# Kernel optimization log

Measured on AMD Instinct MI355X. Metric: run time of the kernel, lower is better.

The kernel has to match this reference:

```python
import jax, jax.numpy as jnp
import numpy as np
from jax import lax


def setup_inputs() -> dict:
    key = jax.random.key(0)
    ks = jax.random.split(key, 12)
    B, T_dec, T_enc, E, H, V = 32, 64, 128, 256, 512, 32000
    s = 0.05
    emb_W = jax.random.normal(ks[0], (V, E), jnp.float32) * s
    emb_W = emb_W.at[0].set(0.0)  # padding_idx=0
    return {
        "dec_X": jax.random.randint(ks[1], (B, T_dec), 0, V, dtype=jnp.int64),
        "enc_output": jax.random.normal(ks[2], (B, T_enc, H), jnp.float32),
        "h0": jax.random.normal(ks[3], (1, B, H), jnp.float32),
        "c0": jax.random.normal(ks[4], (1, B, H), jnp.float32),
        "emb_W": emb_W,
        "W_ih": jax.random.normal(ks[5], (4 * H, E), jnp.float32) * s,
        "W_hh": jax.random.normal(ks[6], (4 * H, H), jnp.float32) * s,
        "b_ih": jax.random.normal(ks[7], (4 * H,), jnp.float32) * s,
        "b_hh": jax.random.normal(ks[8], (4 * H,), jnp.float32) * s,
        "attn_W": jax.random.normal(ks[9], (H, 2 * H), jnp.float32) * s,
        "attn_b": jax.random.normal(ks[10], (H,), jnp.float32) * s,
        "fc_W": jax.random.normal(ks[11], (V, H), jnp.float32) * s,
        "fc_b": jnp.zeros((V,), jnp.float32),
    }


def reference(dec_X, enc_output, h0, c0, emb_W, W_ih, W_hh, b_ih, b_hh,
              attn_W, attn_b, fc_W, fc_b):
    # Embedding lookup for all decoder steps at once; padding_idx=0 -> zero vector.
    emb = emb_W[dec_X] * (dec_X != 0)[..., None].astype(emb_W.dtype)  # [B, T_dec, E]
    h, c = h0[0], c0[0]  # [B, H] (num_layers == 1)
    bias = b_ih + b_hh

    def step(carry, x_t):  # x_t: [B, E]
        h, c = carry
        g = x_t @ W_ih.T + h @ W_hh.T + bias          # [B, 4H]
        i, f, gg, o = jnp.split(g, 4, axis=-1)        # torch gate order i,f,g,o
        c = jax.nn.sigmoid(f) * c + jax.nn.sigmoid(i) * jnp.tanh(gg)
        h = jax.nn.sigmoid(o) * jnp.tanh(c)           # dec_rnn_out
        # dot-product attention over encoder timesteps (softmax over dim 1)
        scores = jnp.einsum('bth,bh->bt', enc_output, h)   # [B, T_enc]
        a = jax.nn.softmax(scores, axis=1)
        c_t = jnp.einsum('bt,bth->bh', a, enc_output)       # [B, H]
        cat = jnp.concatenate([h, c_t], axis=-1)            # [B, 2H]
        out = jnp.tanh(cat @ attn_W.T + attn_b)             # [B, H]
        logits = out @ fc_W.T + fc_b                        # [B, V]
        return (h, c), logits

    (h, c), logits = lax.scan(step, (h, c), jnp.swapaxes(emb, 0, 1))
    output = jnp.swapaxes(logits, 0, 1)  # [B, T_dec, V]
    return output, (h[None], c[None])
```

## Files before the change

### kernel.cpp

```cpp
#include <hip/hip_runtime.h>
#include <cstdint>
#include <cstddef>

typedef unsigned short u16;
typedef short s8v __attribute__((ext_vector_type(8)));
typedef float f4v __attribute__((ext_vector_type(4)));

static __device__ __forceinline__ u16 f2bf(float x) {
  union { float f; uint32_t u; } v; v.f = x;
  uint32_t r = v.u + 0x7fffu + ((v.u >> 16) & 1u);
  return (u16)(r >> 16);
}
static __device__ __forceinline__ float sigm(float x) { return 1.0f / (1.0f + __expf(-x)); }

__global__ void kPrep(const float* __restrict__ fcW, const float* __restrict__ attnW,
                      const float* __restrict__ Wih, const float* __restrict__ bih,
                      const float* __restrict__ bhh, const float* __restrict__ embW,
                      const int* __restrict__ decX,
                      u16* __restrict__ fcWb, u16* __restrict__ attnWb, u16* __restrict__ Wihb,
                      u16* __restrict__ embg, float* __restrict__ biassum,
                      int* __restrict__ syncp) {
  const long NF = 16384000L, NA = 524288L, NW = 524288L, NE = 524288L, NB = 2048L, NS = 1024L;
  const long total = NF + NA + NW + NE + NB + NS;
  for (long i = (long)blockIdx.x * blockDim.x + threadIdx.x; i < total;
       i += (long)gridDim.x * blockDim.x) {
    if (i < NF) {
      fcWb[i] = f2bf(fcW[i]);
    } else if (i < NF + NA) {
      long k = i - NF; attnWb[k] = f2bf(attnW[k]);
    } else if (i < NF + NA + NW) {
      long k = i - NF - NA; Wihb[k] = f2bf(Wih[k]);
    } else if (i < NF + NA + NW + NE) {
      long k = i - NF - NA - NW;
      int row = (int)(k >> 8), e = (int)(k & 255);
      int t = row >> 5, b = row & 31;
      int x = decX[b * 64 + t];
      embg[k] = f2bf(embW[(long)x * 256 + e]);
    } else if (i < NF + NA + NW + NE + NB) {
      long k = i - NF - NA - NW - NE;
      biassum[k] = bih[k] + bhh[k];
    } else {
      long k = i - NF - NA - NW - NE - NB;
      syncp[k] = 0;
    }
  }
}

template <int ACT, int OUTBF>
__global__ __launch_bounds__(256) void kGemm(const u16* __restrict__ A, const u16* __restrict__ Bm,
                                             const float* __restrict__ bias,
                                             float* __restrict__ Cf, u16* __restrict__ Cb,
                                             int N, int K) {
  __shared__ u16 lA[8 * 64 * 8];
  __shared__ u16 lB[8 * 64 * 8];
  const int tid = threadIdx.x;
  const int m0 = blockIdx.x * 128, n0 = blockIdx.y * 128;
  const int lane = tid & 63, wid = tid >> 6;
  const int wm = wid >> 1, wn = wid & 1;
  f4v acc[4][4] = {};
  const int nkt = K >> 5;
  for (int kt = 0; kt < nkt; ++kt) {
    const int k0 = kt << 5;
#pragma unroll
    for (int i = 0; i < 2; ++i) {
      int u = i * 256 + tid;
      int m = u >> 2, q = u & 3;
      uint4 va = *(const uint4*)(A + (size_t)(m0 + m) * K + k0 + q * 8);
      *(uint4*)&lA[(((m >> 4) * 64) + q * 16 + (m & 15)) * 8] = va;
      uint4 vb = *(const uint4*)(Bm + (size_t)(n0 + m) * K + k0 + q * 8);
      *(uint4*)&lB[(((m >> 4) * 64) + q * 16 + (m & 15)) * 8] = vb;
    }
    __syncthreads();
    s8v af[4], bfr[4];
#pragma unroll
    for (int i = 0; i < 4; ++i) af[i] = *(const s8v*)&lA[((wm * 4 + i) * 64 + lane) * 8];
#pragma unroll
    for (int j = 0; j < 4; ++j) bfr[j] = *(const s8v*)&lB[((wn * 4 + j) * 64 + lane) * 8];
#pragma unroll
    for (int i = 0; i < 4; ++i)
#pragma unroll
      for (int j = 0; j < 4; ++j)
        acc[i][j] = __builtin_amdgcn_mfma_f32_16x16x32_bf16(af[i], bfr[j], acc[i][j], 0, 0, 0);
    __syncthreads();
  }
  const int rq = lane >> 4, cl = lane & 15;
#pragma unroll
  for (int j = 0; j < 4; ++j) {
    int col = n0 + wn * 64 + j * 16 + cl;
    float bv = bias[col];
#pragma unroll
    for (int i = 0; i < 4; ++i) {
      int rowb = m0 + wm * 64 + i * 16 + rq * 4;
      f4v v = acc[i][j];
#pragma unroll
      for (int r = 0; r < 4; ++r) {
        float x = v[r] + bv;
        if (ACT) x = tanhf(x);
        size_t off = (size_t)(rowb + r) * N + col;
        if (OUTBF) Cb[off] = f2bf(x); else Cf[off] = x;
      }
    }
  }
}

#define WLDS_H 33024
__global__ __launch_bounds__(256, 1) void kLSTM2(const float* __restrict__ Gpre,
                                                 const float* __restrict__ Whh,
                                                 const float* __restrict__ h0,
                                                 const float* __restrict__ c0,
                                                 float* __restrict__ Hall,
                                                 float* __restrict__ hx,
                                                 float* __restrict__ cx,
                                                 int* __restrict__ syncp) {
  __shared__ float Wl[WLDS_H + 4 * 516];
  __shared__ int srank;
  const int tid = threadIdx.x;

  int xcc;
  asm volatile("s_getreg_b32 %0, hwreg(HW_REG_XCC_ID)" : "=s"(xcc));
  xcc &= 7;
  if (tid == 0) srank = atomicAdd(&syncp[xcc * 64], 1);
  __syncthreads();
  const int rank = srank & 31;
  const int j0 = rank * 16;
  const int b0 = xcc * 4;
  int* cnt = &syncp[(8 + xcc) * 64];

#pragma unroll
  for (int it = 0; it < 32; ++it) {
    int idx = it * 256 + tid;
    int lr = idx >> 7, k4 = idx & 127;
    int gg = lr & 3, jj2 = lr >> 2;
    int grow = gg * 512 + j0 + jj2;
    float4 v = *(const float4*)&Whh[(size_t)grow * 512 + k4 * 4];
    *(float4*)&Wl[lr * 516 + k4 * 4] = v;
  }

  const int jj = tid >> 4;
  const int g  = (tid >> 2) & 3;
  const int bb = tid & 3;
  const int b  = b0 + bb;
  const int j  = j0 + jj;
  const float* wrow = &Wl[(g + 4 * jj) * 516];
  const float* hrow = &Wl[WLDS_H + bb * 516];
  float creg = (g == 0) ? c0[b * 512 + j] : 0.f;

  const float* hsrc = h0;
  __syncthreads();

  for (int t = 0; t < 64; ++t) {
    float gpv = Gpre[((size_t)t * 32 + b) * 2048 + (size_t)g * 512 + j];

#pragma unroll
    for (int it = 0; it < 2; ++it) {
      int idx = it * 256 + tid;
      int hb = idx >> 7, k4 = idx & 127;
      float4 v = *(const float4*)&hsrc[(b0 + hb) * 512 + k4 * 4];
      *(float4*)&Wl[WLDS_H + hb * 516 + k4 * 4] = v;
    }
    __syncthreads();

    float4 a4 = {0.f, 0.f, 0.f, 0.f};
#pragma unroll 8
    for (int k4 = 0; k4 < 128; ++k4) {
      float4 w = *(const float4*)&wrow[k4 * 4];
      float4 h = *(const float4*)&hrow[k4 * 4];
      a4.x += w.x * h.x; a4.y += w.y * h.y; a4.z += w.z * h.z; a4.w += w.w * h.w;
    }
    float pre = (a4.x + a4.z) + (a4.y + a4.w) + gpv;

    float v = (g == 2) ? tanhf(pre) : sigm(pre);
    float fv = __shfl_xor(v, 4, 64);
    float gv = __shfl_xor(v, 8, 64);
    float ov = __shfl_xor(v, 12, 64);
    float* hdst = Hall + (size_t)t * 16384;
    if (g == 0) {
      creg = fv * creg + v * gv;
      float hv = ov * tanhf(creg);
      hdst[b * 512 + j] = hv;
      if (t == 63) { hx[b * 512 + j] = hv; cx[b * 512 + j] = creg; }
    }
    __syncthreads();

    if (t < 63) {
      if (tid == 0) {
        __hip_atomic_fetch_add(cnt, 1, __ATOMIC_RELAXED, __HIP_MEMORY_SCOPE_AGENT);
        const int target = 32 * (t + 1);
        while (__hip_atomic_load(cnt, __ATOMIC_ACQUIRE, __HIP_MEMORY_SCOPE_AGENT) < target)
          __builtin_amdgcn_s_sleep(1);
      }
      __syncthreads();
    }
    hsrc = hdst;
  }
}

__global__ __launch_bounds__(256) void kAttn(const float* __restrict__ Hall, const float* __restrict__ enc,
                                             u16* __restrict__ CAT) {
  const int bx = blockIdx.x;
  const int b = bx >> 3, tg = bx & 7;
  const int tid = threadIdx.x;
  __shared__ float sh[8][516];
  __shared__ float sa[8][132];
  __shared__ float red[8][32];
  for (int tt = 0; tt < 8; ++tt) {
    int t = tg * 8 + tt;
    const float* hr = Hall + ((size_t)t * 32 + b) * 512;
    u16* cr = CAT + ((size_t)(b * 64 + t)) * 1024;
    for (int k = tid; k < 512; k += 256) { float v = hr[k]; sh[tt][k] = v; cr[k] = f2bf(v); }
  }
  __syncthreads();
  {
    const int tl = tid & 7, eb = tid >> 3;
#pragma unroll
    for (int u = 0; u < 4; ++u) {
      int e = eb + u * 32;
      const float* er = enc + ((size_t)b * 128 + e) * 512;
      float a = 0.f;
      for (int k = 0; k < 512; k += 4) {
        float4 ev = *(const float4*)&er[k];
        float4 hv = *(const float4*)&sh[tl][k];
        a += ev.x * hv.x + ev.y * hv.y + ev.z * hv.z + ev.w * hv.w;
      }
      sa[tl][e] = a;
    }
  }
  __syncthreads();
  {
    const int g = tid >> 5, l = tid & 31;
    float mx = -1e30f;
#pragma unroll
    for (int u = 0; u < 4; ++u) mx = fmaxf(mx, sa[g][l + u * 32]);
    red[g][l] = mx;
    __syncthreads();
    if (l == 0) {
      float m2 = -1e30f;
      for (int i = 0; i < 32; ++i) m2 = fmaxf(m2, red[g][i]);
      sa[g][128] = m2;
    }
    __syncthreads();
    float m2 = sa[g][128];
    float s = 0.f;
#pragma unroll
    for (int u = 0; u < 4; ++u) { int e = l + u * 32; float p = __expf(sa[g][e] - m2); sa[g][e] = p; s += p; }
    red[g][l] = s;
    __syncthreads();
    if (l == 0) {
      float s2 = 0.f;
      for (int i = 0; i < 32; ++i) s2 += red[g][i];
      sa[g][129] = 1.0f / s2;
    }
    __syncthreads();
    float inv = sa[g][129];
#pragma unroll
    for (int u = 0; u < 4; ++u) sa[g][l + u * 32] *= inv;
  }
  __syncthreads();
  {
    float a0[8], a1[8];
#pragma unroll
    for (int tt = 0; tt < 8; ++tt) { a0[tt] = 0.f; a1[tt] = 0.f; }
    const float* eb2 = enc + (size_t)b * 128 * 512 + tid * 2;
    for (int e = 0; e < 128; ++e) {
      float2 v = *(const float2*)&eb2[(size_t)e * 512];
#pragma unroll
      for (int tt = 0; tt < 8; ++tt) { float a = sa[tt][e]; a0[tt] += a * v.x; a1[tt] += a * v.y; }
    }
#pragma unroll
    for (int tt = 0; tt < 8; ++tt) {
      int t = tg * 8 + tt;
      u16* cr = CAT + ((size_t)(b * 64 + t)) * 1024 + 512;
      cr[tid * 2] = f2bf(a0[tt]); cr[tid * 2 + 1] = f2bf(a1[tt]);
    }
  }
}

extern "C" void kernel_launch(void* const* d_in, const int* in_sizes, int n_in,
                              void* d_out, int out_size, void* d_ws, size_t ws_size,
                              hipStream_t stream) {
  const int*   decX  = (const int*)d_in[0];
  const float* enc   = (const float*)d_in[1];
  const float* h0    = (const float*)d_in[2];
  const float* c0    = (const float*)d_in[3];
  const float* embW  = (const float*)d_in[4];
  const float* Wih   = (const float*)d_in[5];
  const float* Whh   = (const float*)d_in[6];
  const float* bih   = (const float*)d_in[7];
  const float* bhh   = (const float*)d_in[8];
  const float* attnW = (const float*)d_in[9];
  const float* attnb = (const float*)d_in[10];
  const float* fcW   = (const float*)d_in[11];
  const float* fcb   = (const float*)d_in[12];
  float* out = (float*)d_out;

  char* ws = (char*)d_ws;
  u16*   fcWb    = (u16*)(ws);
  u16*   attnWb  = (u16*)(ws + 32768000);
  u16*   Wihb    = (u16*)(ws + 33816576);
  u16*   embg    = (u16*)(ws + 34865152);
  float* biassum = (float*)(ws + 35913728);
  float* Gpre    = (float*)(ws + 35921920);
  float* Hall    = (float*)(ws + 52699136);
  u16*   CAT     = (u16*)(ws + 56893440);
  u16*   OUTb    = (u16*)(ws + 61087744);
  int*   syncp   = (int*)(ws + 63184896);

  hipLaunchKernelGGL(kPrep, dim3(4096), dim3(256), 0, stream,
                     fcW, attnW, Wih, bih, bhh, embW, decX, fcWb, attnWb, Wihb, embg, biassum,
                     syncp);
  hipLaunchKernelGGL((kGemm<0, 0>), dim3(16, 16), dim3(256), 0, stream,
                     embg, Wihb, biassum, Gpre, (u16*)nullptr, 2048, 256);
  {
    float* hx = out + 65536000L;
    float* cx = out + 65536000L + 16384L;
    const float* gpreA = Gpre; const float* whhA = Whh;
    const float* h0A = h0;     const float* c0A = c0;
    float* hallA = Hall;       int* syncA = syncp;
    void* args[] = {(void*)&gpreA, (void*)&whhA, (void*)&h0A, (void*)&c0A,
                    (void*)&hallA, (void*)&hx, (void*)&cx, (void*)&syncA};
    hipLaunchCooperativeKernel((void*)kLSTM2, dim3(256), dim3(256), args, 0, stream);
  }
  hipLaunchKernelGGL(kAttn, dim3(256), dim3(256), 0, stream, Hall, enc, CAT);
  hipLaunchKernelGGL((kGemm<1, 1>), dim3(16, 4), dim3(256), 0, stream,
                     CAT, attnWb, attnb, (float*)nullptr, OUTb, 512, 1024);
  hipLaunchKernelGGL((kGemm<0, 0>), dim3(16, 250), dim3(256), 0, stream,
                     OUTb, fcWb, fcb, out, (u16*)nullptr, 32000, 512);
}
```

Baseline: 1.027 ms.

## Hold LSTM recurrent weights in registers and split-K reduce via shuffles

The recurrent LSTM kernel now keeps each thread's slice of W_hh (4 gates x 8 float4) in registers instead of LDS. Each thread computes partial dot products for all 16 gate/batch pairs over a strided K slice, and a butterfly shuffle fold reduces them. The goal is to remove the per-step LDS weight reads on the sequential critical path and reuse each h load across four gates. The cost is higher register pressure (128 floats of weights plus 16 accumulators) and extra shuffle instructions.

```diff
diff --git a/kernel.cpp b/kernel.cpp
--- a/kernel.cpp
+++ b/kernel.cpp
@@ -103,8 +103,7 @@
   }
 }
 
-#define WLDS_H 33024
-__global__ __launch_bounds__(256, 1) void kLSTM2(const float* __restrict__ Gpre,
+__global__ __launch_bounds__(256, 1) void kLSTM3(const float* __restrict__ Gpre,
                                                  const float* __restrict__ Whh,
                                                  const float* __restrict__ h0,
                                                  const float* __restrict__ c0,
@@ -112,7 +111,7 @@
                                                  float* __restrict__ hx,
                                                  float* __restrict__ cx,
                                                  int* __restrict__ syncp) {
-  __shared__ float Wl[WLDS_H + 4 * 516];
+  __shared__ float4 hl4[5160];
   __shared__ int srank;
   const int tid = threadIdx.x;
 
@@ -126,59 +125,80 @@
   const int b0 = xcc * 4;
   int* cnt = &syncp[(8 + xcc) * 64];
 
-#pragma unroll
-  for (int it = 0; it < 32; ++it) {
-    int idx = it * 256 + tid;
-    int lr = idx >> 7, k4 = idx & 127;
-    int gg = lr & 3, jj2 = lr >> 2;
-    int grow = gg * 512 + j0 + jj2;
-    float4 v = *(const float4*)&Whh[(size_t)grow * 512 + k4 * 4];
-    *(float4*)&Wl[lr * 516 + k4 * 4] = v;
-  }
-
   const int jj = tid >> 4;
-  const int g  = (tid >> 2) & 3;
-  const int bb = tid & 3;
-  const int b  = b0 + bb;
-  const int j  = j0 + jj;
-  const float* wrow = &Wl[(g + 4 * jj) * 516];
-  const float* hrow = &Wl[WLDS_H + bb * 516];
-  float creg = (g == 0) ? c0[b * 512 + j] : 0.f;
-
-  const float* hsrc = h0;
-  __syncthreads();
+  const int ks = tid & 15;
+  const int g_o = ks >> 2, bb_o = ks & 3;
+  const int b_o = b0 + bb_o;
+  const int j_o = j0 + jj;
+  const bool cellLane = (g_o == 0);
+
+  const float4* W4 = (const float4*)Whh;
+  float4 Wr[4][8];
+#pragma unroll
+  for (int g = 0; g < 4; ++g) {
+    const int row = g * 512 + j0 + jj;
+#pragma unroll
+    for (int i = 0; i < 8; ++i) Wr[g][i] = W4[(size_t)row * 128 + ks + 16 * i];
+  }
+
+  float creg = cellLane ? c0[b_o * 512 + j_o] : 0.f;
+  const float4* hsrc = (const float4*)h0;
 
   for (int t = 0; t < 64; ++t) {
-    float gpv = Gpre[((size_t)t * 32 + b) * 2048 + (size_t)g * 512 + j];
+    float gpv = Gpre[((size_t)t * 32 + b_o) * 2048 + (size_t)g_o * 512 + j_o];
 
 #pragma unroll
     for (int it = 0; it < 2; ++it) {
       int idx = it * 256 + tid;
       int hb = idx >> 7, k4 = idx & 127;
-      float4 v = *(const float4*)&hsrc[(b0 + hb) * 512 + k4 * 4];
-      *(float4*)&Wl[WLDS_H + hb * 516 + k4 * 4] = v;
-    }
-    __syncthreads();
-
-    float4 a4 = {0.f, 0.f, 0.f, 0.f};
-#pragma unroll 8
-    for (int k4 = 0; k4 < 128; ++k4) {
-      float4 w = *(const float4*)&wrow[k4 * 4];
-      float4 h = *(const float4*)&hrow[k4 * 4];
-      a4.x += w.x * h.x; a4.y += w.y * h.y; a4.z += w.z * h.z; a4.w += w.w * h.w;
-    }
-    float pre = (a4.x + a4.z) + (a4.y + a4.w) + gpv;
-
-    float v = (g == 2) ? tanhf(pre) : sigm(pre);
+      hl4[idx] = hsrc[(b0 + hb) * 128 + k4];
+    }
+    __syncthreads();
+
+    float acc[16];
+#pragma unroll
+    for (int p = 0; p < 16; ++p) acc[p] = 0.f;
+#pragma unroll
+    for (int i = 0; i < 8; ++i) {
+      float4 h4[4];
+#pragma unroll
+      for (int bb = 0; bb < 4; ++bb) h4[bb] = hl4[bb * 128 + ks + 16 * i];
+#pragma unroll
+      for (int g = 0; g < 4; ++g) {
+        float4 w = Wr[g][i];
+#pragma unroll
+        for (int bb = 0; bb < 4; ++bb)
+          acc[g * 4 + bb] += w.x * h4[bb].x + w.y * h4[bb].y + w.z * h4[bb].z + w.w * h4[bb].w;
+      }
+    }
+
+#define FOLD_STAGE(OFF, NN)                                        \
+    {                                                              \
+      const bool hi = (ks & OFF) != 0;                             \
+      _Pragma("unroll")                                            \
+      for (int q = 0; q < NN; ++q) {                               \
+        float keepv = hi ? acc[q + NN] : acc[q];                   \
+        float sendv = hi ? acc[q] : acc[q + NN];                   \
+        acc[q] = keepv + __shfl_xor(sendv, OFF, 64);               \
+      }                                                            \
+    }
+    FOLD_STAGE(8, 8)
+    FOLD_STAGE(4, 4)
+    FOLD_STAGE(2, 2)
+    FOLD_STAGE(1, 1)
+#undef FOLD_STAGE
+
+    float pre = acc[0] + gpv;
+    float v = (g_o == 2) ? tanhf(pre) : sigm(pre);
     float fv = __shfl_xor(v, 4, 64);
     float gv = __shfl_xor(v, 8, 64);
     float ov = __shfl_xor(v, 12, 64);
     float* hdst = Hall + (size_t)t * 16384;
-    if (g == 0) {
+    if (cellLane) {
       creg = fv * creg + v * gv;
       float hv = ov * tanhf(creg);
-      hdst[b * 512 + j] = hv;
-      if (t == 63) { hx[b * 512 + j] = hv; cx[b * 512 + j] = creg; }
+      hdst[b_o * 512 + j_o] = hv;
+      if (t == 63) { hx[b_o * 512 + j_o] = hv; cx[b_o * 512 + j_o] = creg; }
     }
     __syncthreads();
 
@@ -191,7 +211,7 @@
       }
       __syncthreads();
     }
-    hsrc = hdst;
+    hsrc = (const float4*)hdst;
   }
 }
 
@@ -318,7 +338,7 @@
     float* hallA = Hall;       int* syncA = syncp;
     void* args[] = {(void*)&gpreA, (void*)&whhA, (void*)&h0A, (void*)&c0A,
                     (void*)&hallA, (void*)&hx, (void*)&cx, (void*)&syncA};
-    hipLaunchCooperativeKernel((void*)kLSTM2, dim3(256), dim3(256), args, 0, stream);
+    hipLaunchCooperativeKernel((void*)kLSTM3, dim3(256), dim3(256), args, 0, stream);
   }
   hipLaunchKernelGGL(kAttn, dim3(256), dim3(256), 0, stream, Hall, enc, CAT);
   hipLaunchKernelGGL((kGemm<1, 1>), dim3(16, 4), dim3(256), 0, stream,
```

New measurement: 937.9 us. 1.1x faster.
